# Kernel optimization log

Hardware: AMD Instinct MI355X
Metric: run time of the kernel (lower is better)

## Reference

```python
import math
import jax, jax.numpy as jnp
import numpy as np

D_MODEL = 1024
N_HEADS = 16
D_HEAD = D_MODEL // N_HEADS
B, T = 2, 2048


def setup_inputs() -> dict:
    key = jax.random.key(0)
    k1, k2, k3, k4, k5 = jax.random.split(key, 5)
    s = 1.0 / math.sqrt(D_MODEL)
    x = jax.random.normal(k1, (B, T, D_MODEL), dtype=jnp.float32)
    w_qkv = jax.random.normal(k2, (D_MODEL, 3 * D_MODEL), dtype=jnp.float32) * s
    b_qkv = jnp.zeros((3 * D_MODEL,), dtype=jnp.float32)
    w_out = jax.random.normal(k3, (D_MODEL, D_MODEL), dtype=jnp.float32) * s
    b_out = jnp.zeros((D_MODEL,), dtype=jnp.float32)
    # causal mask, broadcastable to [B, H, T, T]; 0 -> masked
    attn_mask = jnp.tril(jnp.ones((T, T), dtype=jnp.int32))[None, None]
    return {"x": x, "w_qkv": w_qkv, "b_qkv": b_qkv, "w_out": w_out,
            "b_out": b_out, "attn_mask": attn_mask}


def reference(x, w_qkv, b_qkv, w_out, b_out, attn_mask):
    Bsz, Tlen, C = x.shape
    qkv = x @ w_qkv + b_qkv                       # [B, T, 3C]
    q, k, v = jnp.split(qkv, 3, axis=-1)

    def reshape(t):
        return t.reshape(Bsz, Tlen, N_HEADS, D_HEAD).transpose(0, 2, 1, 3)

    q, k, v = reshape(q), reshape(k), reshape(v)  # [B, H, T, d]
    scores = jnp.einsum("bhqd,bhkd->bhqk", q, k) / math.sqrt(D_HEAD)
    scores = jnp.where(attn_mask == 0, -jnp.inf, scores)
    w = jax.nn.softmax(scores, axis=-1)
    y = jnp.einsum("bhqk,bhkd->bhqd", w, v)       # [B, H, T, d]
    y = y.transpose(0, 2, 1, 3).reshape(Bsz, Tlen, C)
    return y @ w_out + b_out
```

## Files before the change

kernel.cpp:

```cpp
#include <hip/hip_runtime.h>
#include <hip/hip_bf16.h>
#include <stdint.h>


typedef __bf16 bf16_t;
typedef __bf16 bf16x8 __attribute__((ext_vector_type(8)));
typedef __bf16 bf16x4 __attribute__((ext_vector_type(4)));
typedef short  s16x4  __attribute__((ext_vector_type(4)));
typedef float  f32x4  __attribute__((ext_vector_type(4)));

#define SEQ   2048
#define DM    1024
#define NH    16
#define DH    64
#define BATCH 2

__device__ __forceinline__ bf16x8 load8(const bf16_t* p) {
    return *reinterpret_cast<const bf16x8*>(p);
}
__device__ __forceinline__ f32x4 loadf4(const float* p) {
    return *reinterpret_cast<const f32x4*>(p);
}
__device__ __forceinline__ void async16(const bf16_t* g, bf16_t* lds_base) {
    __builtin_amdgcn_global_load_lds(
        (const __attribute__((address_space(1))) void*)g,
        (__attribute__((address_space(3))) void*)lds_base, 16, 0, 0);
}
__device__ __forceinline__ float fast_exp2(float x) {
#if __has_builtin(__builtin_amdgcn_exp2f)
    return __builtin_amdgcn_exp2f(x);
#else
    return __expf(x * 0.69314718056f);
#endif
}
__device__ __forceinline__ int swz(int row, int chunk) {
    return row * 64 + ((chunk ^ (row & 7)) * 8);
}

__device__ __forceinline__ void tcvt_tile(
    const float* __restrict__ w, bf16_t* __restrict__ wT, int N,
    int n0, int k0, bf16_t (*tile)[65])
{
    const int tid = threadIdx.x;
#pragma unroll
    for (int i = 0; i < 4; ++i) {
        const int r = i * 16 + (tid >> 4);
        const int c = (tid & 15) * 4;
        f32x4 v = loadf4(w + (size_t)(k0 + r) * N + n0 + c);
#pragma unroll
        for (int j = 0; j < 4; ++j) tile[c + j][r] = (bf16_t)v[j];
    }
    __syncthreads();
#pragma unroll
    for (int i = 0; i < 4; ++i) {
        const int r = i * 16 + (tid >> 4);
        const int c = (tid & 15) * 4;
        ushort4 v;
        v.x = *(const uint16_t*)&tile[r][c];
        v.y = *(const uint16_t*)&tile[r][c + 1];
        v.z = *(const uint16_t*)&tile[r][c + 2];
        v.w = *(const uint16_t*)&tile[r][c + 3];
        *reinterpret_cast<ushort4*>(wT + (size_t)(n0 + r) * DM + k0 + c) = v;
    }
}

__global__ __launch_bounds__(256) void pre_kernel(
    const float* __restrict__ x, bf16_t* __restrict__ xb,
    const float* __restrict__ w_qkv, bf16_t* __restrict__ wqkvT)
{
    __shared__ bf16_t tile[64][65];
    const int bid = blockIdx.x;
    if (bid < 2048) {
        const int i = (bid * 256 + threadIdx.x) * 8;
        f32x4 a = loadf4(x + i);
        f32x4 b = loadf4(x + i + 4);
        bf16x8 v;
#pragma unroll
        for (int j = 0; j < 4; ++j) { v[j] = (bf16_t)a[j]; v[4 + j] = (bf16_t)b[j]; }
        *reinterpret_cast<bf16x8*>(xb + i) = v;
    } else {
        const int t = bid - 2048;
        tcvt_tile(w_qkv, wqkvT, 3072, (t % 48) * 64, (t / 48) * 64, tile);
    }
}

__global__ __launch_bounds__(256) void tcvt_kernel(
    const float* __restrict__ w, bf16_t* __restrict__ wT, int N)
{
    __shared__ bf16_t tile[64][65];
    tcvt_tile(w, wT, N, blockIdx.x * 64, blockIdx.y * 64, tile);
}

template <typename TA, int MODE, int NT>
__global__ __launch_bounds__(256) void gemm_bt_kernel(
    const TA* __restrict__ A, const bf16_t* __restrict__ BT,
    const float* __restrict__ bias,
    float* __restrict__ outF,
    bf16_t* __restrict__ oq, bf16_t* __restrict__ ok, bf16_t* __restrict__ ov)
{
    constexpr int SAS = (sizeof(TA) == 4) ? 72 : 64;
    constexpr int NB  = NT / 32;
    __shared__ bf16_t sA[128 * SAS];
    __shared__ bf16_t sB[NT * 64];

    const int tid  = threadIdx.x;
    const int lane = tid & 63;
    const int wv   = tid >> 6;
    const int lq   = lane >> 4;
    const int lm   = lane & 15;
    const int wm   = (wv >> 1) * 64;
    const int wn   = (wv & 1) * (NT / 2);

    const int flat = blockIdx.y * gridDim.x + blockIdx.x;
    const int cls  = flat & 7;
    const int q8   = flat >> 3;
    const int mb   = (cls + 8 * (q8 & 3)) * 128;
    const int nb   = (q8 >> 2) * NT;

    const int srow = lane >> 3;
    const int scol = (lane & 7) * 8;
    const int scs  = ((lane & 7) ^ srow) * 8;

    f32x4 acc[4][NB];
#pragma unroll
    for (int a = 0; a < 4; ++a)
#pragma unroll
        for (int b = 0; b < NB; ++b) acc[a][b] = f32x4{0.f, 0.f, 0.f, 0.f};

    for (int it = 0; it < 16; ++it) {
        const int k0 = it * 64;
        if constexpr (sizeof(TA) == 4) {
            const int arow = tid >> 1;
            const int akc  = (tid & 1) * 32;
            const float* g = (const float*)A + (size_t)(mb + arow) * DM + k0 + akc;
            bf16_t* dst = &sA[arow * SAS + akc];
#pragma unroll
            for (int j = 0; j < 4; ++j) {
                f32x4 u0 = loadf4(g + j * 8);
                f32x4 u1 = loadf4(g + j * 8 + 4);
                bf16x8 w;
#pragma unroll
                for (int e = 0; e < 4; ++e) { w[e] = (bf16_t)u0[e]; w[4 + e] = (bf16_t)u1[e]; }
                *reinterpret_cast<bf16x8*>(dst + j * 8) = w;
            }
        } else {
#pragma unroll
            for (int r = 0; r < 4; ++r) {
                const int row = wv * 32 + r * 8 + srow;
                async16((const bf16_t*)A + (size_t)(mb + row) * DM + k0 + scs,
                        &sA[wv * 2048 + r * 512]);
            }
        }
#pragma unroll
        for (int r = 0; r < NT / 32; ++r) {
            const int row = wv * (NT / 4) + r * 8 + srow;
            async16(BT + (size_t)(nb + row) * DM + k0 + scs,
                    &sB[wv * (NT / 4) * 64 + r * 512]);
        }
        __syncthreads();
#pragma unroll
        for (int kh = 0; kh < 2; ++kh) {
            bf16x8 af[4], bfr[NB];
#pragma unroll
            for (int a = 0; a < 4; ++a) {
                if constexpr (sizeof(TA) == 4)
                    af[a] = load8(&sA[(wm + a * 16 + lm) * SAS + kh * 32 + lq * 8]);
                else
                    af[a] = load8(&sA[swz(wm + a * 16 + lm, kh * 4 + lq)]);
            }
#pragma unroll
            for (int b = 0; b < NB; ++b)
                bfr[b] = load8(&sB[swz(wn + b * 16 + lm, kh * 4 + lq)]);
#pragma unroll
            for (int a = 0; a < 4; ++a)
#pragma unroll
                for (int b = 0; b < NB; ++b)
                    acc[a][b] = __builtin_amdgcn_mfma_f32_16x16x32_bf16(
                        af[a], bfr[b], acc[a][b], 0, 0, 0);
        }
        __syncthreads();
    }

#pragma unroll
    for (int b = 0; b < NB; ++b) {
        const int n = nb + wn + b * 16 + lm;
        const float bv = bias[n];
        if (MODE == 0) {
            const int which = n >> 10;
            const int cc = n & 1023;
            const int h  = cc >> 6;
            const int d  = cc & 63;
            if (which == 2) {
#pragma unroll
                for (int a = 0; a < 4; ++a) {
                    const int m0 = mb + wm + a * 16 + lq * 4;
                    const int bb = m0 >> 11;
                    const int t0 = m0 & 2047;
                    bf16x4 w;
#pragma unroll
                    for (int r = 0; r < 4; ++r) w[r] = (bf16_t)(acc[a][b][r] + bv);
                    *reinterpret_cast<bf16x4*>(
                        ov + ((size_t)(bb * NH + h) * DH + d) * SEQ + t0) = w;
                }
            } else {
                bf16_t* dst = (which == 0) ? oq : ok;
#pragma unroll
                for (int a = 0; a < 4; ++a)
#pragma unroll
                    for (int r = 0; r < 4; ++r) {
                        const int m = mb + wm + a * 16 + lq * 4 + r;
                        const int bb = m >> 11;
                        const int t  = m & 2047;
                        dst[((size_t)(bb * NH + h) * SEQ + t) * DH + d] =
                            (bf16_t)(acc[a][b][r] + bv);
                    }
            }
        } else {
#pragma unroll
            for (int a = 0; a < 4; ++a)
#pragma unroll
                for (int r = 0; r < 4; ++r) {
                    const int m = mb + wm + a * 16 + lq * 4 + r;
                    outF[(size_t)m * DM + n] = acc[a][b][r] + bv;
                }
        }
    }
}

__global__ __launch_bounds__(256) void attn_kernel(
    const bf16_t* __restrict__ qbuf, const bf16_t* __restrict__ kbuf,
    const bf16_t* __restrict__ vtbuf, bf16_t* __restrict__ ybuf,
    bf16_t* __restrict__ p1, float* __restrict__ l0buf,
    float* __restrict__ l1buf, int split)
{
    __shared__ bf16_t sK[2][2 * 64 * 64];
    __shared__ bf16_t sVt[2][2 * 64 * 64];

    const int tid  = threadIdx.x;
    const int lane = tid & 63;
    const int wv   = tid >> 6;
    const int lq   = lane >> 4;
    const int lm   = lane & 15;

    const int p    = blockIdx.y * gridDim.x + blockIdx.x;
    const int slot = p >> 3;
    const int bh   = (p & 7) + ((slot & 3) << 3);
    const int uid  = slot >> 2;

    int qi, kt0, ktn, chunk1;
    if (!split)        { qi = 15 - uid;        kt0 = 0;  ktn = 2 * qi + 2;      chunk1 = 0; }
    else if (uid < 9)  { qi = 15 - uid;        kt0 = 0;  ktn = 16;              chunk1 = 0; }
    else if (uid < 17) { qi = 15 - (uid - 9);  kt0 = 16; ktn = 2 * qi + 2 - 16; chunk1 = 1; }
    else               { qi = 6 - (uid - 17);  kt0 = 0;  ktn = 2 * qi + 2;      chunk1 = 0; }
    const bool fin = !split || (!chunk1 && qi < 8);
    const int q_base = qi * 128;
    const int nps = ktn >> 1;

    const size_t hb = (size_t)bh * SEQ * DH;
    const bf16_t* Q  = qbuf + hb;
    const bf16_t* K  = kbuf + hb;
    const bf16_t* VT = vtbuf + hb;

    bf16x8 qf0[2], qf1[2];
#pragma unroll
    for (int ms = 0; ms < 2; ++ms) {
        const bf16_t* p_ = Q + (size_t)(q_base + wv * 32 + ms * 16 + lm) * DH + lq * 8;
        qf0[ms] = load8(p_);
        qf1[ms] = load8(p_ + 32);
    }

    f32x4 o[2][4];
    float ls[2];
#pragma unroll
    for (int ms = 0; ms < 2; ++ms) {
        ls[ms] = 0.f;
#pragma unroll
        for (int dc = 0; dc < 4; ++dc) o[ms][dc] = f32x4{0.f, 0.f, 0.f, 0.f};
    }

    const int srow = lane >> 3;
    const int scs  = ((lane & 7) ^ srow) * 8;

    {
        const int kb0 = kt0 * 64;
#pragma unroll
        for (int hf = 0; hf < 2; ++hf)
#pragma unroll
            for (int r = 0; r < 2; ++r) {
                async16(K + (size_t)(kb0 + hf * 64 + wv * 16 + r * 8 + srow) * DH + scs,
                        &sK[0][hf * 4096 + wv * 1024 + r * 512]);
                async16(VT + (size_t)(wv * 16 + r * 8 + srow) * SEQ + kb0 + hf * 64 + scs,
                        &sVt[0][hf * 4096 + wv * 1024 + r * 512]);
            }
    }
    __syncthreads();

    const float c1 = 0.125f * 1.44269504f;
    const float c2 = 10.0f  * 1.44269504f;

    for (int sp = 0; sp < nps; ++sp) {
        const int cb = sp & 1, nbuf = cb ^ 1;
        if (sp + 1 < nps) {
            const int kb2 = (kt0 + (sp + 1) * 2) * 64;
#pragma unroll
            for (int hf = 0; hf < 2; ++hf)
#pragma unroll
                for (int r = 0; r < 2; ++r) {
                    async16(K + (size_t)(kb2 + hf * 64 + wv * 16 + r * 8 + srow) * DH + scs,
                            &sK[nbuf][hf * 4096 + wv * 1024 + r * 512]);
                    async16(VT + (size_t)(wv * 16 + r * 8 + srow) * SEQ + kb2 + hf * 64 + scs,
                            &sVt[nbuf][hf * 4096 + wv * 1024 + r * 512]);
                }
        }

#pragma unroll
        for (int hf = 0; hf < 2; ++hf) {
            const int kb = (kt0 + sp * 2 + hf) * 64;
            const bf16_t* sKc = &sK[cb][hf * 4096];
            const bf16_t* sVc = &sVt[cb][hf * 4096];

            bf16x8 kf0[4], kf1[4];
#pragma unroll
            for (int c = 0; c < 4; ++c) {
                kf0[c] = load8(&sKc[swz(c * 16 + lm, lq)]);
                kf1[c] = load8(&sKc[swz(c * 16 + lm, lq + 4)]);
            }
            s16x4 vf[4][4];
#pragma unroll
            for (int dc = 0; dc < 4; ++dc)
#pragma unroll
                for (int c = 0; c < 4; ++c)
                    vf[dc][c] = *reinterpret_cast<const s16x4*>(
                        &sVc[swz(dc * 16 + lm, c * 2 + (lq >> 1)) + (lq & 1) * 4]);

#pragma unroll
            for (int ms = 0; ms < 2; ++ms) {
                const int rowlo = wv * 32 + ms * 16;
                if (q_base + rowlo + 15 < kb) continue;

                f32x4 s[4];
                __builtin_amdgcn_s_setprio(1);
#pragma unroll
                for (int c = 0; c < 4; ++c) {
                    f32x4 z = f32x4{0.f, 0.f, 0.f, 0.f};
                    f32x4 t0 = __builtin_amdgcn_mfma_f32_16x16x32_bf16(kf0[c], qf0[ms], z, 0, 0, 0);
                    s[c] = __builtin_amdgcn_mfma_f32_16x16x32_bf16(kf1[c], qf1[ms], t0, 0, 0, 0);
                }
                __builtin_amdgcn_s_setprio(0);

                const int q = q_base + rowlo + lm;
                float p4[4][4];
                if (kb + 63 > q_base + rowlo) {
#pragma unroll
                    for (int c = 0; c < 4; ++c)
#pragma unroll
                        for (int r = 0; r < 4; ++r) {
                            const int key = kb + c * 16 + lq * 4 + r;
                            float t = (key <= q) ? fmaf(s[c][r], c1, -c2) : -1e30f;
                            p4[c][r] = fast_exp2(t);
                        }
                } else {
#pragma unroll
                    for (int c = 0; c < 4; ++c)
#pragma unroll
                        for (int r = 0; r < 4; ++r)
                            p4[c][r] = fast_exp2(fmaf(s[c][r], c1, -c2));
                }
                float lsum = 0.f;
#pragma unroll
                for (int c = 0; c < 4; ++c)
                    lsum += (p4[c][0] + p4[c][1]) + (p4[c][2] + p4[c][3]);
                ls[ms] += lsum;

                s16x4 pf[4];
#pragma unroll
                for (int c = 0; c < 4; ++c) {
                    bf16x4 v;
#pragma unroll
                    for (int r = 0; r < 4; ++r) v[r] = (bf16_t)p4[c][r];
                    pf[c] = __builtin_bit_cast(s16x4, v);
                }

                __builtin_amdgcn_s_setprio(1);
#pragma unroll
                for (int dc = 0; dc < 4; ++dc)
#pragma unroll
                    for (int c = 0; c < 4; ++c)
                        o[ms][dc] = __builtin_amdgcn_mfma_f32_16x16x16bf16_1k(
                            vf[dc][c], pf[c], o[ms][dc], 0, 0, 0);
                __builtin_amdgcn_s_setprio(0);
            }
        }

        __syncthreads();
    }

    __syncthreads();
    bf16_t* sT = &sK[0][0];
    const int b = bh >> 4;
    const int h = bh & 15;
#pragma unroll
    for (int ms = 0; ms < 2; ++ms) {
        float l = ls[ms];
        l += __shfl_xor(l, 16);
        l += __shfl_xor(l, 32);
        const float inv = fin ? (1.0f / l) : 1.0f;
        if (!fin && lq == 0) {
            const int q = q_base + wv * 32 + ms * 16 + lm;
            float* lb = chunk1 ? l1buf : l0buf;
            lb[bh * 1024 + (q - 1024)] = l;
        }
#pragma unroll
        for (int dc = 0; dc < 4; ++dc)
#pragma unroll
            for (int r = 0; r < 4; ++r)
                sT[wv * 1152 + lm * 72 + dc * 16 + lq * 4 + r] =
                    (bf16_t)(o[ms][dc][r] * inv);
        const int t = q_base + wv * 32 + ms * 16 + (lane & 15);
        const bf16_t* src = &sT[wv * 1152 + (lane & 15) * 72 + (lane >> 4) * 16];
        bf16x8 y0 = load8(src);
        bf16x8 y1 = load8(src + 8);
        bf16_t* dst;
        if (chunk1)
            dst = p1 + ((size_t)(bh * 1024 + (t - 1024))) * 64 + (lane >> 4) * 16;
        else
            dst = ybuf + ((size_t)(b * SEQ + t)) * DM + h * DH + (lane >> 4) * 16;
        *reinterpret_cast<bf16x8*>(dst)     = y0;
        *reinterpret_cast<bf16x8*>(dst + 8) = y1;
    }
}

__global__ __launch_bounds__(256) void post_kernel(
    bf16_t* __restrict__ yb, const bf16_t* __restrict__ p1,
    const float* __restrict__ l0, const float* __restrict__ l1,
    const float* __restrict__ w_out, bf16_t* __restrict__ woutT)
{
    __shared__ bf16_t tile[64][65];
    const int bid = blockIdx.x;
    if (bid < 1024) {
        const int idx = bid * 256 + threadIdx.x;
        const int d8  = (idx & 7) * 8;
        const int row = idx >> 3;
        const int ql  = row & 1023;
        const int bh  = row >> 10;
        const int q   = 1024 + ql;
        const int b   = bh >> 4, h = bh & 15;
        const float inv = 1.0f / (l0[row] + l1[row]);
        bf16_t* yp = yb + ((size_t)(b * SEQ + q)) * DM + h * DH + d8;
        const bf16_t* pp = p1 + (size_t)row * 64 + d8;
        bf16x8 a = load8(yp), c = load8(pp);
        bf16x8 oo;
#pragma unroll
        for (int j = 0; j < 8; ++j)
            oo[j] = (bf16_t)(((float)a[j] + (float)c[j]) * inv);
        *reinterpret_cast<bf16x8*>(yp) = oo;
    } else {
        const int t = bid - 1024;
        tcvt_tile(w_out, woutT, 1024, (t % 16) * 64, (t / 16) * 64, tile);
    }
}

extern "C" void kernel_launch(void* const* d_in, const int* in_sizes, int n_in,
                              void* d_out, int out_size, void* d_ws, size_t ws_size,
                              hipStream_t stream)
{
    const float* x     = (const float*)d_in[0];
    const float* w_qkv = (const float*)d_in[1];
    const float* b_qkv = (const float*)d_in[2];
    const float* w_out = (const float*)d_in[3];
    const float* b_out = (const float*)d_in[4];
    float* out = (float*)d_out;

    char* ws = (char*)d_ws;
    bf16_t* qb = (bf16_t*)(ws);
    bf16_t* kb = (bf16_t*)(ws + (8u << 20));
    bf16_t* vb = (bf16_t*)(ws + (16u << 20));
    bf16_t* yb = (bf16_t*)(ws + (24u << 20));
    bf16_t* woutT = qb;

    const bool bigws = (ws_size >= ((size_t)38 << 20));

    if (bigws) {
        bf16_t* xb    = yb;
        bf16_t* wqkvT = (bf16_t*)(ws + (32u << 20));
        pre_kernel<<<dim3(2048 + 768), dim3(256), 0, stream>>>(x, xb, w_qkv, wqkvT);
        gemm_bt_kernel<bf16_t, 0, 128><<<dim3(3072 / 128, 4096 / 128), dim3(256), 0, stream>>>(
            xb, wqkvT, b_qkv, nullptr, qb, kb, vb);

        bf16_t* p1 = (bf16_t*)(ws + (32u << 20));
        float*  l0 = (float*)(ws + (36u << 20));
        float*  l1 = (float*)(ws + (36u << 20) + (128u << 10));
        attn_kernel<<<dim3(24, BATCH * NH), dim3(256), 0, stream>>>(
            qb, kb, vb, yb, p1, l0, l1, 1);
        post_kernel<<<dim3(1024 + 256), dim3(256), 0, stream>>>(
            yb, p1, l0, l1, w_out, woutT);
    } else {
        bf16_t* wqkvT = yb;
        tcvt_kernel<<<dim3(3072 / 64, 1024 / 64), dim3(256), 0, stream>>>(w_qkv, wqkvT, 3072);
        gemm_bt_kernel<float, 0, 128><<<dim3(3072 / 128, 4096 / 128), dim3(256), 0, stream>>>(
            x, wqkvT, b_qkv, nullptr, qb, kb, vb);
        attn_kernel<<<dim3(16, 32), dim3(256), 0, stream>>>(
            qb, kb, vb, yb, yb, nullptr, nullptr, 0);
        tcvt_kernel<<<dim3(1024 / 64, 1024 / 64), dim3(256), 0, stream>>>(w_out, woutT, 1024);
    }

    gemm_bt_kernel<bf16_t, 1, 64><<<dim3(1024 / 64, 4096 / 128), dim3(256), 0, stream>>>(
        yb, woutT, b_out, out, nullptr, nullptr, nullptr);
}
```

Before: 188.0 us.

## Replace QKV GEMM with 256x256 8-wave pipelined kernel; drop attention setprio

Adds a new 512-thread QKV projection kernel with 256x256 output tiles. It stages A and B through a 4-slot LDS ring with async global-to-LDS loads, and interleaves prefetch with MFMA quarter-steps under explicit vmcnt waits and barriers. The goal is higher reuse per tile and less exposed memory latency than the previous 128x128 GEMM. It also removes the s_setprio hints around the MFMAs in the attention kernel. The bigger tile uses 128 KB of LDS and many accumulator registers, so occupancy drops and only 192 blocks are launched, which may leave compute units idle.

```diff
diff --git a/kernel.cpp b/kernel.cpp
--- a/kernel.cpp
+++ b/kernel.cpp
@@ -91,6 +91,151 @@
     tcvt_tile(w, wT, N, blockIdx.x * 64, blockIdx.y * 64, tile);
 }
 
+__global__ __launch_bounds__(512) void gemm8p_kernel(
+    const bf16_t* __restrict__ A, const bf16_t* __restrict__ BT,
+    const float* __restrict__ bias,
+    bf16_t* __restrict__ oq, bf16_t* __restrict__ ok, bf16_t* __restrict__ ov)
+{
+    __shared__ bf16_t sA[4 * 128 * 64];
+    __shared__ bf16_t sB[4 * 128 * 64];
+
+    const int tid  = threadIdx.x;
+    const int lane = tid & 63;
+    const int wv   = tid >> 6;
+    const int wr   = wv >> 2;
+    const int wc   = wv & 3;
+    const int lq   = lane >> 4;
+    const int lm   = lane & 15;
+
+    const int flat = blockIdx.y * gridDim.x + blockIdx.x;
+    const int cls  = flat & 7;
+    const int q8   = flat >> 3;
+    const int mb   = (cls + 8 * (q8 & 1)) * 256;
+    const int nb   = (q8 >> 1) * 256;
+
+    const int scs  = ((lane & 7) ^ (lane >> 3)) * 8;
+
+    auto stageA = [&](int tt, int h) {
+        const int slot = (2 * tt + h) & 3;
+        const int k0 = tt * 64;
+#pragma unroll
+        for (int j = 0; j < 2; ++j) {
+            const int row = h * 128 + wv * 8 + (lane >> 3) + j * 64;
+            async16(A + (size_t)(mb + row) * DM + k0 + scs,
+                    &sA[slot * 8192 + (wv * 8 + j * 64) * 64]);
+        }
+    };
+    auto stageB = [&](int tt, int h) {
+        const int slot = (2 * tt + h) & 3;
+        const int k0 = tt * 64;
+#pragma unroll
+        for (int j = 0; j < 2; ++j) {
+            const int row = h * 128 + wv * 8 + (lane >> 3) + j * 64;
+            async16(BT + (size_t)(nb + row) * DM + k0 + scs,
+                    &sB[slot * 8192 + (wv * 8 + j * 64) * 64]);
+        }
+    };
+
+    f32x4 acc[8][4];
+#pragma unroll
+    for (int f = 0; f < 8; ++f)
+#pragma unroll
+        for (int nf = 0; nf < 4; ++nf) acc[f][nf] = f32x4{0.f, 0.f, 0.f, 0.f};
+
+    stageB(0, 0); stageB(0, 1);
+    stageA(0, 0); stageA(0, 1);
+    stageB(1, 0); stageB(1, 1);
+    asm volatile("s_waitcnt vmcnt(4)" ::: "memory");
+    __builtin_amdgcn_sched_barrier(0);
+    __builtin_amdgcn_s_barrier();
+
+    for (int t = 0; t < 16; ++t) {
+        const bf16_t* sAc = &sA[((2 * t + wr) & 3) * 8192];
+        const bf16_t* sBc = &sB[((2 * t + (wc >> 1)) & 3) * 8192];
+        bf16x8 bf[4][2];
+#pragma unroll
+        for (int q = 0; q < 4; ++q) {
+            if (q == 0 && t + 1 < 16) stageA(t + 1, 0);
+            if (q == 1 && t + 1 < 16) stageA(t + 1, 1);
+            if (q == 1 && t + 2 < 16) stageB(t + 2, 0);
+            if (q == 2 && t + 2 < 16) stageB(t + 2, 1);
+
+            if (q == 0) {
+#pragma unroll
+                for (int nf = 0; nf < 4; ++nf)
+#pragma unroll
+                    for (int kh = 0; kh < 2; ++kh)
+                        bf[nf][kh] = load8(
+                            &sBc[swz((wc & 1) * 64 + nf * 16 + lm, kh * 4 + lq)]);
+            }
+            bf16x8 af[2][2];
+#pragma unroll
+            for (int j = 0; j < 2; ++j)
+#pragma unroll
+                for (int kh = 0; kh < 2; ++kh)
+                    af[j][kh] = load8(
+                        &sAc[swz((2 * q + j) * 16 + lm, kh * 4 + lq)]);
+
+            if (q == 3) {
+                if (t < 14) {
+                    asm volatile("s_waitcnt vmcnt(4)" ::: "memory");
+                } else if (t < 15) {
+                    asm volatile("s_waitcnt vmcnt(0)" ::: "memory");
+                }
+                __builtin_amdgcn_sched_barrier(0);
+            }
+            __builtin_amdgcn_s_barrier();
+
+            __builtin_amdgcn_s_setprio(1);
+#pragma unroll
+            for (int kh = 0; kh < 2; ++kh)
+#pragma unroll
+                for (int j = 0; j < 2; ++j)
+#pragma unroll
+                    for (int nf = 0; nf < 4; ++nf)
+                        acc[2 * q + j][nf] = __builtin_amdgcn_mfma_f32_16x16x32_bf16(
+                            af[j][kh], bf[nf][kh], acc[2 * q + j][nf], 0, 0, 0);
+            __builtin_amdgcn_s_setprio(0);
+            __builtin_amdgcn_s_barrier();
+        }
+    }
+
+#pragma unroll
+    for (int nf = 0; nf < 4; ++nf) {
+        const int n = nb + wc * 64 + nf * 16 + lm;
+        const float bv = bias[n];
+        const int which = n >> 10;
+        const int cc = n & 1023;
+        const int h  = cc >> 6;
+        const int d  = cc & 63;
+        if (which == 2) {
+#pragma unroll
+            for (int f = 0; f < 8; ++f) {
+                const int m0 = mb + wr * 128 + f * 16 + lq * 4;
+                const int bb = m0 >> 11;
+                const int t0 = m0 & 2047;
+                bf16x4 w;
+#pragma unroll
+                for (int r = 0; r < 4; ++r) w[r] = (bf16_t)(acc[f][nf][r] + bv);
+                *reinterpret_cast<bf16x4*>(
+                    ov + ((size_t)(bb * NH + h) * DH + d) * SEQ + t0) = w;
+            }
+        } else {
+            bf16_t* dst = (which == 0) ? oq : ok;
+#pragma unroll
+            for (int f = 0; f < 8; ++f)
+#pragma unroll
+                for (int r = 0; r < 4; ++r) {
+                    const int m = mb + wr * 128 + f * 16 + lq * 4 + r;
+                    const int bb = m >> 11;
+                    const int t  = m & 2047;
+                    dst[((size_t)(bb * NH + h) * SEQ + t) * DH + d] =
+                        (bf16_t)(acc[f][nf][r] + bv);
+                }
+        }
+    }
+}
+
 template <typename TA, int MODE, int NT>
 __global__ __launch_bounds__(256) void gemm_bt_kernel(
     const TA* __restrict__ A, const bf16_t* __restrict__ BT,
@@ -118,7 +263,6 @@
     const int nb   = (q8 >> 2) * NT;
 
     const int srow = lane >> 3;
-    const int scol = (lane & 7) * 8;
     const int scs  = ((lane & 7) ^ srow) * 8;
 
     f32x4 acc[4][NB];
@@ -339,14 +483,12 @@
                 if (q_base + rowlo + 15 < kb) continue;
 
                 f32x4 s[4];
-                __builtin_amdgcn_s_setprio(1);
 #pragma unroll
                 for (int c = 0; c < 4; ++c) {
                     f32x4 z = f32x4{0.f, 0.f, 0.f, 0.f};
                     f32x4 t0 = __builtin_amdgcn_mfma_f32_16x16x32_bf16(kf0[c], qf0[ms], z, 0, 0, 0);
                     s[c] = __builtin_amdgcn_mfma_f32_16x16x32_bf16(kf1[c], qf1[ms], t0, 0, 0, 0);
                 }
-                __builtin_amdgcn_s_setprio(0);
 
                 const int q = q_base + rowlo + lm;
                 float p4[4][4];
@@ -381,14 +523,12 @@
                     pf[c] = __builtin_bit_cast(s16x4, v);
                 }
 
-                __builtin_amdgcn_s_setprio(1);
 #pragma unroll
                 for (int dc = 0; dc < 4; ++dc)
 #pragma unroll
                     for (int c = 0; c < 4; ++c)
                         o[ms][dc] = __builtin_amdgcn_mfma_f32_16x16x16bf16_1k(
                             vf[dc][c], pf[c], o[ms][dc], 0, 0, 0);
-                __builtin_amdgcn_s_setprio(0);
             }
         }
 
@@ -484,8 +624,8 @@
         bf16_t* xb    = yb;
         bf16_t* wqkvT = (bf16_t*)(ws + (32u << 20));
         pre_kernel<<<dim3(2048 + 768), dim3(256), 0, stream>>>(x, xb, w_qkv, wqkvT);
-        gemm_bt_kernel<bf16_t, 0, 128><<<dim3(3072 / 128, 4096 / 128), dim3(256), 0, stream>>>(
-            xb, wqkvT, b_qkv, nullptr, qb, kb, vb);
+        gemm8p_kernel<<<dim3(3072 / 256, 4096 / 256), dim3(512), 0, stream>>>(
+            xb, wqkvT, b_qkv, qb, kb, vb);
 
         bf16_t* p1 = (bf16_t*)(ws + (32u << 20));
         float*  l0 = (float*)(ws + (36u << 20));
```

Result: slower. 201.0 us (+6.9%).
